# Performance work log

Measured on AMD Instinct MI355X. Metric: run time of the kernel, lower is better.

## Reference

```python
import jax, jax.numpy as jnp
import numpy as np


def setup_inputs() -> dict:
    key = jax.random.key(0)
    ks = jax.random.split(key, 8)
    B, M, C, H, W = 2, 16, 256, 64, 64
    T = 1024  # transformer_dim
    return {
        "transformer_output": jax.random.normal(ks[0], (B, T), dtype=jnp.float32),
        "residual_maps": jax.random.normal(ks[1], (B, M, C, H, W), dtype=jnp.float32),
        "Wq": jax.random.normal(ks[2], (C, T), dtype=jnp.float32) * 0.02,
        "bq": jnp.zeros((C,), dtype=jnp.float32),
        "Wk": jax.random.normal(ks[3], (C, C), dtype=jnp.float32) * 0.02,
        "bk": jnp.zeros((C,), dtype=jnp.float32),
        "Wv": jax.random.normal(ks[4], (C, C), dtype=jnp.float32) * 0.02,
        "bv": jnp.zeros((C,), dtype=jnp.float32),
    }


def reference(transformer_output, residual_maps, Wq, bq, Wk, bk, Wv, bv):
    # residual_maps: [B, M, C, H, W]; single query per batch element.
    B, M, C, H, W = residual_maps.shape
    scale = C ** (-0.5)
    # Linear query projection: [B, C]
    q = transformer_output @ Wq.T + bq
    # 1x1 conv == per-pixel channel matmul: [B, M, C, H, W]
    keys = jnp.einsum("oc,bmchw->bmohw", Wk, residual_maps) + bk[None, None, :, None, None]
    values = jnp.einsum("oc,bmchw->bmohw", Wv, residual_maps) + bv[None, None, :, None, None]
    # Single-query dot-product scores per (map, pixel): [B, M, H, W]
    scores = jnp.einsum("bc,bmchw->bmhw", q, keys) * scale
    # Temporal softmax over num_maps at each spatial position
    probs = jax.nn.softmax(scores, axis=1)
    # Softmax-weighted sum of value maps: [B, C, H, W]
    out = jnp.einsum("bmhw,bmchw->bchw", probs, values)
    return out
```

## Files before the change

kernel.cpp:

```cpp
#include <hip/hip_runtime.h>

#define SCALE 0.0625f

__global__ __launch_bounds__(256) void prep1_kernel(
    const float* __restrict__ TO,
    const float* __restrict__ Wq,
    const float* __restrict__ bq,
    const float* __restrict__ Wv,
    float* __restrict__ qbuf,
    float* __restrict__ WvT)
{
    const int blk = blockIdx.x;
    const int t   = threadIdx.x;
    if (blk < 16) {
        const int b    = blk >> 3;
        const int rblk = blk & 7;
        const int wv = t >> 6, l = t & 63;
        const float4* Wq4 = (const float4*)Wq;
        const float4* TO4 = (const float4*)TO;
        for (int rr = 0; rr < 8; ++rr) {
            const int c = rblk * 32 + wv * 8 + rr;
            float acc = 0.f;
#pragma unroll
            for (int i = 0; i < 4; ++i) {
                float4 wq = Wq4[c * 256 + i * 64 + l];
                float4 tv = TO4[b * 256 + i * 64 + l];
                acc = fmaf(wq.x, tv.x, acc);
                acc = fmaf(wq.y, tv.y, acc);
                acc = fmaf(wq.z, tv.z, acc);
                acc = fmaf(wq.w, tv.w, acc);
            }
#pragma unroll
            for (int mask = 1; mask < 64; mask <<= 1)
                acc += __shfl_xor(acc, mask, 64);
            if (l == 0) qbuf[b * 256 + c] = acc + bq[c];
        }
    } else {
        const int idx = blk - 16;
        const int r0 = (idx >> 2) * 64;
        const int c0 = (idx & 3) * 64;
        __shared__ float tile[64][65];
#pragma unroll
        for (int i = 0; i < 16; ++i) {
            int ii = t + 256 * i;
            int r = ii >> 6, c = ii & 63;
            tile[r][c] = Wv[(r0 + r) * 256 + (c0 + c)];
        }
        __syncthreads();
#pragma unroll
        for (int i = 0; i < 16; ++i) {
            int ii = t + 256 * i;
            int rT = ii >> 6, cT = ii & 63;
            WvT[(c0 + rT) * 256 + (r0 + cT)] = tile[cT][rT];
        }
    }
}

__global__ __launch_bounds__(256) void prep2_kernel(
    const float* __restrict__ qbuf,
    const float* __restrict__ Wk,
    float* __restrict__ qks)
{
    const int blk = blockIdx.x;
    const int t   = threadIdx.x;
    const int b = blk >> 3, j = blk & 7;
    const int col = t & 31, chunk = t >> 5;
    const int cp = j * 32 + col;
    float partial = 0.f;
#pragma unroll 8
    for (int cc = 0; cc < 32; ++cc) {
        const int c = chunk * 32 + cc;
        partial = fmaf(qbuf[b * 256 + c], Wk[c * 256 + cp], partial);
    }
    __shared__ float r2[8][32];
    r2[chunk][col] = partial;
    __syncthreads();
    if (t < 32) {
        float s = 0.f;
#pragma unroll
        for (int k = 0; k < 8; ++k) s += r2[k][t];
        qks[b * 256 + j * 32 + t] = SCALE * s;
    }
}

__global__ __launch_bounds__(256) void main_kernel(
    const float* __restrict__ X,
    const float* __restrict__ qks,
    const float* __restrict__ WvT,
    const float* __restrict__ bv,
    float* __restrict__ out)
{
    const int t   = threadIdx.x;
    const int blk = blockIdx.x;
    const int b   = blk >> 8;
    const int hw0 = (blk & 255) << 4;
    const int p4  = t & 3;
    const int cg  = t >> 2;
    const int l   = t & 63;
    const int wv  = t >> 6;

    float qk[4];
#pragma unroll
    for (int k = 0; k < 4; ++k) qk[k] = qks[b * 256 + cg + 64 * k];

    float4 wx[4];
#pragma unroll
    for (int k = 0; k < 4; ++k) wx[k] = make_float4(0.f, 0.f, 0.f, 0.f);
    float lsum[4] = {0.f, 0.f, 0.f, 0.f};

    __shared__ __align__(16) float4 red[2][4][4];
    __shared__ __align__(16) float slab2[256 * 20];

    const float4* X4 = (const float4*)X;
    const int pixbase = (hw0 >> 2) + p4;
    const int base0   = (b * 16) * 262144 + pixbase;
    const int cstep[4] = {(cg) * 1024, (cg + 64) * 1024,
                          (cg + 128) * 1024, (cg + 192) * 1024};

    float4 v[3][4];
#pragma unroll
    for (int k = 0; k < 4; ++k) v[0][k] = X4[base0 + 0 * 262144 + cstep[k]];
#pragma unroll
    for (int k = 0; k < 4; ++k) v[1][k] = X4[base0 + 1 * 262144 + cstep[k]];

#pragma unroll
    for (int m = 0; m < 16; ++m) {
        const int cur = m % 3;
        const int nxt = (m + 2) % 3;
        if (m < 14) {
#pragma unroll
            for (int k = 0; k < 4; ++k)
                v[nxt][k] = X4[base0 + (m + 2) * 262144 + cstep[k]];
        }
        float sx = 0.f, sy = 0.f, sz = 0.f, sw = 0.f;
#pragma unroll
        for (int k = 0; k < 4; ++k) {
            sx = fmaf(qk[k], v[cur][k].x, sx);
            sy = fmaf(qk[k], v[cur][k].y, sy);
            sz = fmaf(qk[k], v[cur][k].z, sz);
            sw = fmaf(qk[k], v[cur][k].w, sw);
        }
#pragma unroll
        for (int mask = 4; mask < 64; mask <<= 1) {
            sx += __shfl_xor(sx, mask, 64);
            sy += __shfl_xor(sy, mask, 64);
            sz += __shfl_xor(sz, mask, 64);
            sw += __shfl_xor(sw, mask, 64);
        }
        const int buf = m & 1;
        if (l < 4) red[buf][wv][l] = make_float4(sx, sy, sz, sw);
        __syncthreads();
        const float4 r0 = red[buf][0][p4];
        const float4 r1 = red[buf][1][p4];
        const float4 r2_ = red[buf][2][p4];
        const float4 r3 = red[buf][3][p4];
        float w[4];
        w[0] = __expf(r0.x + r1.x + r2_.x + r3.x);
        w[1] = __expf(r0.y + r1.y + r2_.y + r3.y);
        w[2] = __expf(r0.z + r1.z + r2_.z + r3.z);
        w[3] = __expf(r0.w + r1.w + r2_.w + r3.w);
#pragma unroll
        for (int i = 0; i < 4; ++i) lsum[i] += w[i];
#pragma unroll
        for (int k = 0; k < 4; ++k) {
            wx[k].x = fmaf(w[0], v[cur][k].x, wx[k].x);
            wx[k].y = fmaf(w[1], v[cur][k].y, wx[k].y);
            wx[k].z = fmaf(w[2], v[cur][k].z, wx[k].z);
            wx[k].w = fmaf(w[3], v[cur][k].w, wx[k].w);
        }
    }

    float inv[4];
#pragma unroll
    for (int i = 0; i < 4; ++i) inv[i] = 1.0f / lsum[i];
#pragma unroll
    for (int k = 0; k < 4; ++k) {
        const int c = cg + 64 * k;
        *(float4*)&slab2[c * 20 + 4 * p4] =
            make_float4(wx[k].x * inv[0], wx[k].y * inv[1],
                        wx[k].z * inv[2], wx[k].w * inv[3]);
    }
    __syncthreads();

    const int cq = t & 63;
    const int pq = t >> 6;
    const float4* WvT4 = (const float4*)WvT;
    const float4  bvv  = ((const float4*)bv)[cq];
    float acc[4][4];
#pragma unroll
    for (int pi = 0; pi < 4; ++pi) {
        acc[0][pi] = bvv.x; acc[1][pi] = bvv.y;
        acc[2][pi] = bvv.z; acc[3][pi] = bvv.w;
    }
#pragma unroll 4
    for (int o = 0; o < 256; ++o) {
        const float4 wv4 = WvT4[o * 64 + cq];
        const float4 xv  = *(const float4*)&slab2[o * 20 + 4 * pq];
        acc[0][0] = fmaf(wv4.x, xv.x, acc[0][0]);
        acc[0][1] = fmaf(wv4.x, xv.y, acc[0][1]);
        acc[0][2] = fmaf(wv4.x, xv.z, acc[0][2]);
        acc[0][3] = fmaf(wv4.x, xv.w, acc[0][3]);
        acc[1][0] = fmaf(wv4.y, xv.x, acc[1][0]);
        acc[1][1] = fmaf(wv4.y, xv.y, acc[1][1]);
        acc[1][2] = fmaf(wv4.y, xv.z, acc[1][2]);
        acc[1][3] = fmaf(wv4.y, xv.w, acc[1][3]);
        acc[2][0] = fmaf(wv4.z, xv.x, acc[2][0]);
        acc[2][1] = fmaf(wv4.z, xv.y, acc[2][1]);
        acc[2][2] = fmaf(wv4.z, xv.z, acc[2][2]);
        acc[2][3] = fmaf(wv4.z, xv.w, acc[2][3]);
        acc[3][0] = fmaf(wv4.w, xv.x, acc[3][0]);
        acc[3][1] = fmaf(wv4.w, xv.y, acc[3][1]);
        acc[3][2] = fmaf(wv4.w, xv.z, acc[3][2]);
        acc[3][3] = fmaf(wv4.w, xv.w, acc[3][3]);
    }
    const int obase = b * 256 * 4096 + hw0 + 4 * pq;
#pragma unroll
    for (int ci = 0; ci < 4; ++ci) {
        const int c = 4 * cq + ci;
        *(float4*)&out[obase + c * 4096] =
            make_float4(acc[ci][0], acc[ci][1], acc[ci][2], acc[ci][3]);
    }
}

extern "C" void kernel_launch(void* const* d_in, const int* in_sizes, int n_in,
                              void* d_out, int out_size, void* d_ws, size_t ws_size,
                              hipStream_t stream) {
    const float* TO = (const float*)d_in[0];
    const float* X  = (const float*)d_in[1];
    const float* Wq = (const float*)d_in[2];
    const float* bq = (const float*)d_in[3];
    const float* Wk = (const float*)d_in[4];
    const float* Wv = (const float*)d_in[6];
    const float* bv = (const float*)d_in[7];
    float* out = (float*)d_out;
    float* ws  = (float*)d_ws;

    float* qbuf = ws;
    float* qks  = ws + 512;
    float* WvT  = ws + 1024;

    hipLaunchKernelGGL(prep1_kernel, dim3(32), dim3(256), 0, stream,
                       TO, Wq, bq, Wv, qbuf, WvT);
    hipLaunchKernelGGL(prep2_kernel, dim3(16), dim3(256), 0, stream,
                       qbuf, Wk, qks);
    hipLaunchKernelGGL(main_kernel, dim3(512), dim3(256), 0, stream,
                       X, qks, WvT, bv, out);
}
```

Baseline: 246.4 us.

## Use single-wave blocks with bf16 MFMA for value projection

Shrinks the main kernel to one 64-thread wavefront per block, so each thread holds 16 channel float4s and the score reduction needs only shuffles, with no LDS exchange or block barrier per map. The final Wv projection becomes bf16 MFMA 16x16x32 ops, using a bf16 copy of Wv made in prep1 in place of the fp32 transpose. Block indices are also swizzled across XCDs. The trade-offs are bf16 precision loss, heavy register pressure, and only 512 single-wave blocks, so there is less latency hiding for the dominant X stream.

```diff
diff --git a/kernel.cpp b/kernel.cpp
--- a/kernel.cpp
+++ b/kernel.cpp
@@ -1,6 +1,15 @@
 #include <hip/hip_runtime.h>
 
 #define SCALE 0.0625f
+
+typedef __attribute__((ext_vector_type(4))) float f32x4;
+typedef __attribute__((ext_vector_type(8))) short s16x8;
+
+__device__ __forceinline__ unsigned short f2bf(float x) {
+    unsigned u = __float_as_uint(x);
+    u = u + 0x7FFF + ((u >> 16) & 1);
+    return (unsigned short)(u >> 16);
+}
 
 __global__ __launch_bounds__(256) void prep1_kernel(
     const float* __restrict__ TO,
@@ -8,7 +17,7 @@
     const float* __restrict__ bq,
     const float* __restrict__ Wv,
     float* __restrict__ qbuf,
-    float* __restrict__ WvT)
+    unsigned short* __restrict__ WvB)
 {
     const int blk = blockIdx.x;
     const int t   = threadIdx.x;
@@ -37,21 +46,14 @@
         }
     } else {
         const int idx = blk - 16;
-        const int r0 = (idx >> 2) * 64;
-        const int c0 = (idx & 3) * 64;
-        __shared__ float tile[64][65];
-#pragma unroll
-        for (int i = 0; i < 16; ++i) {
-            int ii = t + 256 * i;
-            int r = ii >> 6, c = ii & 63;
-            tile[r][c] = Wv[(r0 + r) * 256 + (c0 + c)];
-        }
-        __syncthreads();
-#pragma unroll
-        for (int i = 0; i < 16; ++i) {
-            int ii = t + 256 * i;
-            int rT = ii >> 6, cT = ii & 63;
-            WvT[(c0 + rT) * 256 + (r0 + cT)] = tile[cT][rT];
+#pragma unroll
+        for (int i = 0; i < 4; ++i) {
+            const int e = idx * 4096 + i * 1024 + t * 4;
+            const float4 f = ((const float4*)Wv)[e >> 2];
+            ushort4 o;
+            o.x = f2bf(f.x); o.y = f2bf(f.y);
+            o.z = f2bf(f.z); o.w = f2bf(f.w);
+            *(ushort4*)(WvB + e) = o;
         }
     }
 }
@@ -83,62 +85,55 @@
     }
 }
 
-__global__ __launch_bounds__(256) void main_kernel(
+__global__ __launch_bounds__(64, 1) void main_kernel(
     const float* __restrict__ X,
     const float* __restrict__ qks,
-    const float* __restrict__ WvT,
+    const unsigned short* __restrict__ WvB,
     const float* __restrict__ bv,
     float* __restrict__ out)
 {
     const int t   = threadIdx.x;
     const int blk = blockIdx.x;
-    const int b   = blk >> 8;
-    const int hw0 = (blk & 255) << 4;
+    const int pb  = ((blk & 7) << 6) | (blk >> 3);
+    const int b   = pb >> 8;
+    const int hw0 = (pb & 255) << 4;
     const int p4  = t & 3;
     const int cg  = t >> 2;
-    const int l   = t & 63;
-    const int wv  = t >> 6;
-
-    float qk[4];
-#pragma unroll
-    for (int k = 0; k < 4; ++k) qk[k] = qks[b * 256 + cg + 64 * k];
-
-    float4 wx[4];
-#pragma unroll
-    for (int k = 0; k < 4; ++k) wx[k] = make_float4(0.f, 0.f, 0.f, 0.f);
+
+    __shared__ float slab[256 * 20];
+
+    float qk[16];
+#pragma unroll
+    for (int k = 0; k < 16; ++k) qk[k] = qks[b * 256 + cg + 16 * k];
+
+    const float4* X4 = (const float4*)X;
+    const int base0 = (b * 16) * 262144 + (hw0 >> 2) + p4;
+
+    float4 v[2][16];
+    float4 wx[16];
+#pragma unroll
+    for (int k = 0; k < 16; ++k) wx[k] = make_float4(0.f, 0.f, 0.f, 0.f);
     float lsum[4] = {0.f, 0.f, 0.f, 0.f};
 
-    __shared__ __align__(16) float4 red[2][4][4];
-    __shared__ __align__(16) float slab2[256 * 20];
-
-    const float4* X4 = (const float4*)X;
-    const int pixbase = (hw0 >> 2) + p4;
-    const int base0   = (b * 16) * 262144 + pixbase;
-    const int cstep[4] = {(cg) * 1024, (cg + 64) * 1024,
-                          (cg + 128) * 1024, (cg + 192) * 1024};
-
-    float4 v[3][4];
-#pragma unroll
-    for (int k = 0; k < 4; ++k) v[0][k] = X4[base0 + 0 * 262144 + cstep[k]];
-#pragma unroll
-    for (int k = 0; k < 4; ++k) v[1][k] = X4[base0 + 1 * 262144 + cstep[k]];
+#pragma unroll
+    for (int k = 0; k < 16; ++k)
+        v[0][k] = X4[base0 + (cg + 16 * k) * 1024];
 
 #pragma unroll
     for (int m = 0; m < 16; ++m) {
-        const int cur = m % 3;
-        const int nxt = (m + 2) % 3;
-        if (m < 14) {
-#pragma unroll
-            for (int k = 0; k < 4; ++k)
-                v[nxt][k] = X4[base0 + (m + 2) * 262144 + cstep[k]];
+        const int buf = m & 1, nxt = buf ^ 1;
+        if (m < 15) {
+#pragma unroll
+            for (int k = 0; k < 16; ++k)
+                v[nxt][k] = X4[base0 + (m + 1) * 262144 + (cg + 16 * k) * 1024];
         }
         float sx = 0.f, sy = 0.f, sz = 0.f, sw = 0.f;
 #pragma unroll
-        for (int k = 0; k < 4; ++k) {
-            sx = fmaf(qk[k], v[cur][k].x, sx);
-            sy = fmaf(qk[k], v[cur][k].y, sy);
-            sz = fmaf(qk[k], v[cur][k].z, sz);
-            sw = fmaf(qk[k], v[cur][k].w, sw);
+        for (int k = 0; k < 16; ++k) {
+            sx = fmaf(qk[k], v[buf][k].x, sx);
+            sy = fmaf(qk[k], v[buf][k].y, sy);
+            sz = fmaf(qk[k], v[buf][k].z, sz);
+            sw = fmaf(qk[k], v[buf][k].w, sw);
         }
 #pragma unroll
         for (int mask = 4; mask < 64; mask <<= 1) {
@@ -147,78 +142,61 @@
             sz += __shfl_xor(sz, mask, 64);
             sw += __shfl_xor(sw, mask, 64);
         }
-        const int buf = m & 1;
-        if (l < 4) red[buf][wv][l] = make_float4(sx, sy, sz, sw);
-        __syncthreads();
-        const float4 r0 = red[buf][0][p4];
-        const float4 r1 = red[buf][1][p4];
-        const float4 r2_ = red[buf][2][p4];
-        const float4 r3 = red[buf][3][p4];
-        float w[4];
-        w[0] = __expf(r0.x + r1.x + r2_.x + r3.x);
-        w[1] = __expf(r0.y + r1.y + r2_.y + r3.y);
-        w[2] = __expf(r0.z + r1.z + r2_.z + r3.z);
-        w[3] = __expf(r0.w + r1.w + r2_.w + r3.w);
-#pragma unroll
-        for (int i = 0; i < 4; ++i) lsum[i] += w[i];
-#pragma unroll
-        for (int k = 0; k < 4; ++k) {
-            wx[k].x = fmaf(w[0], v[cur][k].x, wx[k].x);
-            wx[k].y = fmaf(w[1], v[cur][k].y, wx[k].y);
-            wx[k].z = fmaf(w[2], v[cur][k].z, wx[k].z);
-            wx[k].w = fmaf(w[3], v[cur][k].w, wx[k].w);
-        }
-    }
-
-    float inv[4];
-#pragma unroll
-    for (int i = 0; i < 4; ++i) inv[i] = 1.0f / lsum[i];
-#pragma unroll
-    for (int k = 0; k < 4; ++k) {
-        const int c = cg + 64 * k;
-        *(float4*)&slab2[c * 20 + 4 * p4] =
-            make_float4(wx[k].x * inv[0], wx[k].y * inv[1],
-                        wx[k].z * inv[2], wx[k].w * inv[3]);
+        const float w0 = __expf(sx), w1 = __expf(sy);
+        const float w2 = __expf(sz), w3 = __expf(sw);
+        lsum[0] += w0; lsum[1] += w1; lsum[2] += w2; lsum[3] += w3;
+#pragma unroll
+        for (int k = 0; k < 16; ++k) {
+            wx[k].x = fmaf(w0, v[buf][k].x, wx[k].x);
+            wx[k].y = fmaf(w1, v[buf][k].y, wx[k].y);
+            wx[k].z = fmaf(w2, v[buf][k].z, wx[k].z);
+            wx[k].w = fmaf(w3, v[buf][k].w, wx[k].w);
+        }
+    }
+
+    const float i0 = 1.0f / lsum[0], i1 = 1.0f / lsum[1];
+    const float i2 = 1.0f / lsum[2], i3 = 1.0f / lsum[3];
+#pragma unroll
+    for (int k = 0; k < 16; ++k) {
+        *(float4*)&slab[(cg + 16 * k) * 20 + 4 * p4] =
+            make_float4(wx[k].x * i0, wx[k].y * i1, wx[k].z * i2, wx[k].w * i3);
     }
     __syncthreads();
 
-    const int cq = t & 63;
-    const int pq = t >> 6;
-    const float4* WvT4 = (const float4*)WvT;
-    const float4  bvv  = ((const float4*)bv)[cq];
-    float acc[4][4];
-#pragma unroll
-    for (int pi = 0; pi < 4; ++pi) {
-        acc[0][pi] = bvv.x; acc[1][pi] = bvv.y;
-        acc[2][pi] = bvv.z; acc[3][pi] = bvv.w;
-    }
-#pragma unroll 4
-    for (int o = 0; o < 256; ++o) {
-        const float4 wv4 = WvT4[o * 64 + cq];
-        const float4 xv  = *(const float4*)&slab2[o * 20 + 4 * pq];
-        acc[0][0] = fmaf(wv4.x, xv.x, acc[0][0]);
-        acc[0][1] = fmaf(wv4.x, xv.y, acc[0][1]);
-        acc[0][2] = fmaf(wv4.x, xv.z, acc[0][2]);
-        acc[0][3] = fmaf(wv4.x, xv.w, acc[0][3]);
-        acc[1][0] = fmaf(wv4.y, xv.x, acc[1][0]);
-        acc[1][1] = fmaf(wv4.y, xv.y, acc[1][1]);
-        acc[1][2] = fmaf(wv4.y, xv.z, acc[1][2]);
-        acc[1][3] = fmaf(wv4.y, xv.w, acc[1][3]);
-        acc[2][0] = fmaf(wv4.z, xv.x, acc[2][0]);
-        acc[2][1] = fmaf(wv4.z, xv.y, acc[2][1]);
-        acc[2][2] = fmaf(wv4.z, xv.z, acc[2][2]);
-        acc[2][3] = fmaf(wv4.z, xv.w, acc[2][3]);
-        acc[3][0] = fmaf(wv4.w, xv.x, acc[3][0]);
-        acc[3][1] = fmaf(wv4.w, xv.y, acc[3][1]);
-        acc[3][2] = fmaf(wv4.w, xv.z, acc[3][2]);
-        acc[3][3] = fmaf(wv4.w, xv.w, acc[3][3]);
-    }
-    const int obase = b * 256 * 4096 + hw0 + 4 * pq;
-#pragma unroll
-    for (int ci = 0; ci < 4; ++ci) {
-        const int c = 4 * cq + ci;
-        *(float4*)&out[obase + c * 4096] =
-            make_float4(acc[ci][0], acc[ci][1], acc[ci][2], acc[ci][3]);
+    const int px   = t & 15;
+    const int quad = t >> 4;
+
+    f32x4 acc[16];
+#pragma unroll
+    for (int tt = 0; tt < 16; ++tt) {
+#pragma unroll
+        for (int r = 0; r < 4; ++r)
+            acc[tt][r] = bv[16 * tt + quad * 4 + r];
+    }
+
+#pragma unroll
+    for (int ks = 0; ks < 8; ++ks) {
+        s16x8 bfr;
+#pragma unroll
+        for (int j = 0; j < 8; ++j)
+            bfr[j] = (short)f2bf(slab[(ks * 32 + quad * 8 + j) * 20 + px]);
+#pragma unroll
+        for (int tt = 0; tt < 16; ++tt) {
+            const s16x8 afr =
+                *(const s16x8*)(WvB + (16 * tt + px) * 256 + ks * 32 + quad * 8);
+            acc[tt] = __builtin_amdgcn_mfma_f32_16x16x32_bf16(afr, bfr, acc[tt],
+                                                              0, 0, 0);
+        }
+    }
+
+    const int obase = b * 256 * 4096 + hw0;
+#pragma unroll
+    for (int tt = 0; tt < 16; ++tt) {
+#pragma unroll
+        for (int r = 0; r < 4; ++r) {
+            const int co = 16 * tt + quad * 4 + r;
+            out[obase + co * 4096 + px] = acc[tt][r];
+        }
     }
 }
 
@@ -235,14 +213,14 @@
     float* out = (float*)d_out;
     float* ws  = (float*)d_ws;
 
-    float* qbuf = ws;
-    float* qks  = ws + 512;
-    float* WvT  = ws + 1024;
+    float*          qbuf = ws;
+    float*          qks  = ws + 512;
+    unsigned short* WvB  = (unsigned short*)(ws + 1024);
 
     hipLaunchKernelGGL(prep1_kernel, dim3(32), dim3(256), 0, stream,
-                       TO, Wq, bq, Wv, qbuf, WvT);
+                       TO, Wq, bq, Wv, qbuf, WvB);
     hipLaunchKernelGGL(prep2_kernel, dim3(16), dim3(256), 0, stream,
                        qbuf, Wk, qks);
-    hipLaunchKernelGGL(main_kernel, dim3(512), dim3(256), 0, stream,
-                       X, qks, WvT, bv, out);
-}
+    hipLaunchKernelGGL(main_kernel, dim3(512), dim3(64), 0, stream,
+                       X, qks, WvB, bv, out);
+}
```

After: 242.0 us. No clear change (-1.8%).
